# Kernel optimization log

Measured on AMD Instinct MI355X. Metric: run time of the kernel, lower is better.

The kernel has to match this reference:

```python
import jax, jax.numpy as jnp
import numpy as np

NUM_M = 512
NUM_T = 64
MAX_STEPS = 20
TAU = 1.0


def setup_inputs() -> dict:
    key = jax.random.key(0)
    ks = jax.random.split(key, 10)
    num_m, num_t = NUM_M, NUM_T
    inp = {
        "v_src": jax.random.normal(ks[0], (1, num_m), jnp.float32),
        "v_target": jax.random.normal(ks[1], (1, num_m), jnp.float32),
        # small-magnitude generators so matrix_exp stays well-conditioned
        "omegas": jax.random.normal(ks[2], (num_t, num_m, num_m), jnp.float32) * 0.01,
        "W1": jax.random.normal(ks[3], (2 * num_m, 256), jnp.float32) * (1.0 / np.sqrt(2 * num_m)),
        "b1": jnp.zeros((256,), jnp.float32),
        "W2": jax.random.normal(ks[4], (256, 128), jnp.float32) * (1.0 / np.sqrt(256)),
        "b2": jnp.zeros((128,), jnp.float32),
        "W3": jax.random.normal(ks[5], (128, num_t), jnp.float32) * (1.0 / np.sqrt(128)),
        "b3": jnp.zeros((num_t,), jnp.float32),
        # pre-sampled gumbel noise, one draw per step: [max_steps, B, num_t]
        "gumbel_noise": jax.random.gumbel(ks[6], (MAX_STEPS, 1, num_t), jnp.float32),
    }
    return inp


def reference(v_src, v_target, omegas, W1, b1, W2, b2, W3, b3, gumbel_noise):
    tgt_idx = jnp.argmax(v_target, axis=-1)  # [B]

    def mlp(x):
        h = jax.nn.relu(x @ W1 + b1)
        h = jax.nn.relu(h @ W2 + b2)
        return h @ W3 + b3  # [B, num_t]

    batched_expm = jax.vmap(jax.scipy.linalg.expm)

    def step(carry, g):
        v, done = carry  # v: [B, num_m], done: [B] bool
        x = jnp.concatenate([v, v_target], axis=-1)        # [B, 2*num_m]
        logits = mlp(x)                                     # [B, num_t]
        # gumbel_softmax(tau=1.0, hard=False)
        soft = jax.nn.softmax((logits + g) / TAU, axis=-1)
        omega_k = jnp.einsum('bt,tmk->bmk', soft, omegas)   # [B, m, m]
        R_k = batched_expm(omega_k)                         # [B, m, m]
        v_new = jnp.einsum('bmk,bk->bm', R_k, v)            # [B, m]
        # freeze state and zero-pad logits once the target marking was reached
        v_out = jnp.where(done[:, None], v, v_new)
        logits_out = jnp.where(done[:, None], jnp.zeros_like(logits), logits)
        done_new = done | (jnp.argmax(v_new, axis=-1) == tgt_idx)
        return (v_out, done_new), logits_out

    done0 = jnp.zeros((v_src.shape[0],), bool)
    (v_final, _), logits_seq = jax.lax.scan(step, (v_src, done0), gumbel_noise)
    # logits_seq: [max_steps, B, num_t]; B==1 -> [max_steps, num_t] (torch squeeze(0))
    return v_final, logits_seq[:, 0, :]
```

## Files before the change

kernel.cpp:

```cpp
#include <hip/hip_runtime.h>
#include <hip/hip_fp16.h>


#define NBLK 256
#define NTHR 512
#define NSTEP 20
#define NTAY 3
#define RBUF 4

typedef unsigned long long ull;

#define XW(buf, i) (X + ((((buf) << 8) + (i)) << 3))

__device__ __forceinline__ float wredsum(float p) {
#pragma unroll
  for (int off = 32; off > 0; off >>= 1) p += __shfl_xor(p, off, 64);
  return p;
}

__device__ __forceinline__ void publish2(ull* w, float v0, float v1, unsigned int tag2) {
  unsigned int u0 = (__float_as_uint(v0) & ~3u) | tag2;
  ull x = (ull)u0 | ((ull)__float_as_uint(v1) << 32);
  __hip_atomic_store(w, x, __ATOMIC_RELAXED, __HIP_MEMORY_SCOPE_AGENT);
}

__device__ __forceinline__ float2 poll2(ull* w, unsigned int tag2) {
  int it = 0;
  for (;;) {
    ull x = __hip_atomic_load(w, __ATOMIC_RELAXED, __HIP_MEMORY_SCOPE_AGENT);
    if ((unsigned int)(x & 3u) == tag2) {
      float2 r;
      r.x = __uint_as_float((unsigned int)x);
      r.y = __uint_as_float((unsigned int)(x >> 32));
      return r;
    }
    if (it == 0)      __builtin_amdgcn_s_sleep(1);
    else if (it == 1) __builtin_amdgcn_s_sleep(2);
    else              __builtin_amdgcn_s_sleep(4);
    if (it < 2) ++it;
  }
}

__global__ __launch_bounds__(NTHR) void petri_kernel(
    const float* __restrict__ vsrc, const float* __restrict__ vtgt,
    const float* __restrict__ omg,  const float* __restrict__ W1,
    const float* __restrict__ b1,   const float* __restrict__ W2,
    const float* __restrict__ b2,   const float* __restrict__ W3,
    const float* __restrict__ b3,   const float* __restrict__ gum,
    ull* __restrict__ X, float* __restrict__ out) {
  __shared__ __half2 oh[64 * 512];
  __shared__ float A0_s[512], A1_s[512];
  __shared__ float v_loc[512], tgt_s[512], w_s[512];
  __shared__ float w1c_s[1024];
  __shared__ float gum_s[NSTEP * 64];
  __shared__ float b2_s[128], b3_s[64];
  __shared__ float soft_s[64], h1_s[256], h2_s[128];
  __shared__ float redp[512];
  __shared__ float rf8[8];
  __shared__ int   ri8[8];
  __shared__ float acc2[2];
  __shared__ int   bc[1];

  const int b = blockIdx.x, tid = threadIdx.x;
  const int wv = tid >> 6, ln = tid & 63;

  v_loc[tid] = vsrc[tid];
  tgt_s[tid] = vtgt[tid];
  w1c_s[tid] = W1[tid * 256 + b];
  w1c_s[tid + 512] = W1[(tid + 512) * 256 + b];
  for (int i = tid; i < NSTEP * 64; i += NTHR) gum_s[i] = gum[i];
  if (tid >= 512 - 128) {
    int j = tid - (512 - 128);
    b2_s[j] = b2[j];
    if (j < 64) b3_s[j] = b3[j];
  }
  float w2r[64];
  {
    const int o = tid & 127, q = tid >> 7;
    const float* p = W2 + ((q << 6) * 128) + o;
#pragma unroll
    for (int i = 0; i < 64; ++i) w2r[i] = p[i * 128];
  }
  float w3r[16];
  {
    const int o = tid & 63, q = tid >> 6;
    const float* p = W3 + ((q << 4) * 64) + o;
#pragma unroll
    for (int i = 0; i < 16; ++i) w3r[i] = p[i * 64];
  }
  {
    const float* base0 = omg + (b << 10) + tid;
#pragma unroll 4
    for (int t = 0; t < 64; ++t) {
      float x0 = base0[t * 262144];
      float x1 = base0[t * 262144 + 512];
      oh[t * 512 + tid] = __floats2half2_rn(x0, x1);
    }
  }
  __syncthreads();

  int tgtIdx;
  {
    float v = tgt_s[tid]; int ix = tid;
#pragma unroll
    for (int off = 32; off > 0; off >>= 1) {
      float ov = __shfl_xor(v, off, 64); int oi = __shfl_xor(ix, off, 64);
      if (ov > v || (ov == v && oi < ix)) { v = ov; ix = oi; }
    }
    if (ln == 0) { rf8[wv] = v; ri8[wv] = ix; }
    __syncthreads();
    if (tid == 0) {
      float bv = rf8[0]; int bix = ri8[0];
      for (int q = 1; q < 8; ++q)
        if (rf8[q] > bv || (rf8[q] == bv && ri8[q] < bix)) { bv = rf8[q]; bix = ri8[q]; }
      bc[0] = bix;
    }
    __syncthreads();
    tgtIdx = bc[0];
    __syncthreads();
  }

  int d = 0;
  int r = 0;

  for (int s = 0; s < NSTEP; ++s) {
    if (d) {
      if (b == 0 && tid < 64) out[512 + s * 64 + tid] = 0.0f;
      continue;
    }

    {
      const int buf = r & (RBUF - 1);
      const unsigned int tg = (unsigned int)((r >> 2) & 3);
      float p = fmaf(v_loc[tid], w1c_s[tid], tgt_s[tid] * w1c_s[tid + 512]);
      p = wredsum(p);
      if (ln == 0) rf8[wv] = p;
      __syncthreads();
      if (tid == 0) {
        float a = b1[b];
        for (int q = 0; q < 8; ++q) a += rf8[q];
        float h = fmaxf(a, 0.f);
        publish2(XW(buf, b), h, h, tg);
      }
      if (tid < 256) h1_s[tid] = poll2(XW(buf, tid), tg).x;
      __syncthreads();
      ++r;
    }

    {
      const int q = tid >> 7;
      float a = 0.f;
      const float* hp = h1_s + (q << 6);
#pragma unroll
      for (int i = 0; i < 64; ++i) a = fmaf(hp[i], w2r[i], a);
      redp[tid] = a;
    }
    __syncthreads();
    if (tid < 128) {
      float rr = redp[tid] + redp[tid + 128] + redp[tid + 256] + redp[tid + 384] + b2_s[tid];
      h2_s[tid] = fmaxf(rr, 0.f);
    }
    __syncthreads();
    {
      const int q = tid >> 6;
      float a = 0.f;
      const float* hp = h2_s + (q << 4);
#pragma unroll
      for (int i = 0; i < 16; ++i) a = fmaf(hp[i], w3r[i], a);
      redp[tid] = a;
    }
    __syncthreads();
    if (tid < 64) {
      float a = b3_s[tid];
#pragma unroll
      for (int q = 0; q < 8; ++q) a += redp[tid + (q << 6)];
      float lg = a + gum_s[s * 64 + tid];
      float mx = lg;
#pragma unroll
      for (int off = 32; off > 0; off >>= 1) mx = fmaxf(mx, __shfl_xor(mx, off, 64));
      float e = __expf(lg - mx);
      float sm = e;
#pragma unroll
      for (int off = 32; off > 0; off >>= 1) sm += __shfl_xor(sm, off, 64);
      soft_s[tid] = e / sm;
      if (b == 0) out[512 + s * 64 + tid] = a;
    }
    __syncthreads();

    {
      float a0 = 0.f, a1 = 0.f;
#pragma unroll 8
      for (int t = 0; t < 64; ++t) {
        float2 xy = __half22float2(oh[t * 512 + tid]);
        float sv = soft_s[t];
        a0 = fmaf(sv, xy.x, a0);
        a1 = fmaf(sv, xy.y, a1);
      }
      A0_s[tid] = a0; A1_s[tid] = a1;
    }
    __syncthreads();

    {
      const int buf = r & (RBUF - 1);
      const unsigned int tg = (unsigned int)((r >> 2) & 3);
      const float* Ar = (tid < 256) ? A0_s : A1_s;
      const int j = tid & 255;
      float p = fmaf(Ar[j], v_loc[j], Ar[j + 256] * v_loc[j + 256]);
      p = wredsum(p);
      if (ln == 0) rf8[wv] = p;
      __syncthreads();
      if (tid == 0) {
        float s0 = rf8[0] + rf8[1] + rf8[2] + rf8[3];
        float s1 = rf8[4] + rf8[5] + rf8[6] + rf8[7];
        acc2[0] = v_loc[(b << 1)] + s0;
        acc2[1] = v_loc[(b << 1) + 1] + s1;
        publish2(XW(buf, b), s0, s1, tg);
      }
      if (tid < 256) {
        float2 g = poll2(XW(buf, tid), tg);
        w_s[(tid << 1)] = g.x;
        w_s[(tid << 1) + 1] = g.y;
      }
      __syncthreads();
      ++r;
    }

    for (int n = 2; n <= NTAY; ++n) {
      const int buf = r & (RBUF - 1);
      const unsigned int tg = (unsigned int)((r >> 2) & 3);
      const float* Ar = (tid < 256) ? A0_s : A1_s;
      const int j = tid & 255;
      float p = fmaf(Ar[j], w_s[j], Ar[j + 256] * w_s[j + 256]);
      p = wredsum(p);
      if (ln == 0) rf8[wv] = p;
      __syncthreads();
      if (tid == 0) {
        const float inv = 1.0f / (float)n;
        float s0 = (rf8[0] + rf8[1] + rf8[2] + rf8[3]) * inv;
        float s1 = (rf8[4] + rf8[5] + rf8[6] + rf8[7]) * inv;
        acc2[0] += s0; acc2[1] += s1;
        float p0 = (n < NTAY) ? s0 : acc2[0];
        float p1 = (n < NTAY) ? s1 : acc2[1];
        publish2(XW(buf, b), p0, p1, tg);
      }
      if (n < NTAY) {
        if (tid < 256) {
          float2 g = poll2(XW(buf, tid), tg);
          w_s[(tid << 1)] = g.x;
          w_s[(tid << 1) + 1] = g.y;
        }
        __syncthreads();
        ++r;
      } else {
        if (tid < 256) {
          float2 g = poll2(XW(buf, tid), tg);
          v_loc[(tid << 1)] = g.x;
          v_loc[(tid << 1) + 1] = g.y;
        }
        __syncthreads();
        float v = v_loc[tid]; int ix = tid;
#pragma unroll
        for (int off = 32; off > 0; off >>= 1) {
          float ov = __shfl_xor(v, off, 64); int oi = __shfl_xor(ix, off, 64);
          if (ov > v || (ov == v && oi < ix)) { v = ov; ix = oi; }
        }
        if (ln == 0) { rf8[wv] = v; ri8[wv] = ix; }
        __syncthreads();
        if (tid == 0) {
          float bv = rf8[0]; int bix = ri8[0];
          for (int q = 1; q < 8; ++q)
            if (rf8[q] > bv || (rf8[q] == bv && ri8[q] < bix)) { bv = rf8[q]; bix = ri8[q]; }
          bc[0] = (bix == tgtIdx) ? 1 : 0;
        }
        __syncthreads();
        if (bc[0]) d = 1;
        __syncthreads();
        ++r;
      }
    }
  }

  if (b == 0) out[tid] = v_loc[tid];
}

extern "C" void kernel_launch(void* const* d_in, const int* in_sizes, int n_in,
                              void* d_out, int out_size, void* d_ws, size_t ws_size,
                              hipStream_t stream) {
  (void)in_sizes; (void)n_in; (void)out_size; (void)ws_size;
  petri_kernel<<<dim3(NBLK), dim3(NTHR), 0, stream>>>(
      (const float*)d_in[0], (const float*)d_in[1], (const float*)d_in[2],
      (const float*)d_in[3], (const float*)d_in[4], (const float*)d_in[5],
      (const float*)d_in[6], (const float*)d_in[7], (const float*)d_in[8],
      (const float*)d_in[9], (ull*)d_ws, (float*)d_out);
}
```

Before: 364.6 us.

## Run Taylor-series exchange rounds in a single wavefront to drop block barriers

The three Taylor-series matvec and all-to-all exchange rounds, plus the final argmax, now run inside wavefront 0 alone. The state vector is held in registers, eight entries per lane, and each lane polls four slots at once, so the per-round __syncthreads and the LDS reduction through tid 0 go away. The constant target half of the first MLP layer is computed once before the loop, and the omega preload now uses float4 loads. In exchange, each round's dot product is done by 64 lanes instead of 512, and the other wavefronts sit idle during the critical serial exchange path.

```diff
diff --git a/kernel.cpp b/kernel.cpp
--- a/kernel.cpp
+++ b/kernel.cpp
@@ -16,6 +16,16 @@
 #pragma unroll
   for (int off = 32; off > 0; off >>= 1) p += __shfl_xor(p, off, 64);
   return p;
+}
+
+__device__ __forceinline__ void wredsum2(float& p0, float& p1) {
+#pragma unroll
+  for (int off = 32; off > 0; off >>= 1) {
+    float t0 = __shfl_xor(p0, off, 64);
+    float t1 = __shfl_xor(p1, off, 64);
+    p0 += t0;
+    p1 += t1;
+  }
 }
 
 __device__ __forceinline__ void publish2(ull* w, float v0, float v1, unsigned int tag2) {
@@ -41,6 +51,27 @@
   }
 }
 
+__device__ __forceinline__ void poll8(ull* w0, unsigned int tg, float* o) {
+  ull x0 = 0, x1 = 0, x2 = 0, x3 = 0;
+  bool g0 = false, g1 = false, g2 = false, g3 = false;
+  int it = 0;
+  for (;;) {
+    if (!g0) { ull x = __hip_atomic_load(w0,      __ATOMIC_RELAXED, __HIP_MEMORY_SCOPE_AGENT); if ((unsigned int)(x & 3u) == tg) { x0 = x; g0 = true; } }
+    if (!g1) { ull x = __hip_atomic_load(w0 + 8,  __ATOMIC_RELAXED, __HIP_MEMORY_SCOPE_AGENT); if ((unsigned int)(x & 3u) == tg) { x1 = x; g1 = true; } }
+    if (!g2) { ull x = __hip_atomic_load(w0 + 16, __ATOMIC_RELAXED, __HIP_MEMORY_SCOPE_AGENT); if ((unsigned int)(x & 3u) == tg) { x2 = x; g2 = true; } }
+    if (!g3) { ull x = __hip_atomic_load(w0 + 24, __ATOMIC_RELAXED, __HIP_MEMORY_SCOPE_AGENT); if ((unsigned int)(x & 3u) == tg) { x3 = x; g3 = true; } }
+    if (g0 && g1 && g2 && g3) break;
+    if (it == 0)      __builtin_amdgcn_s_sleep(1);
+    else if (it == 1) __builtin_amdgcn_s_sleep(2);
+    else              __builtin_amdgcn_s_sleep(4);
+    if (it < 2) ++it;
+  }
+  o[0] = __uint_as_float((unsigned int)x0); o[1] = __uint_as_float((unsigned int)(x0 >> 32));
+  o[2] = __uint_as_float((unsigned int)x1); o[3] = __uint_as_float((unsigned int)(x1 >> 32));
+  o[4] = __uint_as_float((unsigned int)x2); o[5] = __uint_as_float((unsigned int)(x2 >> 32));
+  o[6] = __uint_as_float((unsigned int)x3); o[7] = __uint_as_float((unsigned int)(x3 >> 32));
+}
+
 __global__ __launch_bounds__(NTHR) void petri_kernel(
     const float* __restrict__ vsrc, const float* __restrict__ vtgt,
     const float* __restrict__ omg,  const float* __restrict__ W1,
@@ -49,8 +80,10 @@
     const float* __restrict__ b3,   const float* __restrict__ gum,
     ull* __restrict__ X, float* __restrict__ out) {
   __shared__ __half2 oh[64 * 512];
-  __shared__ float A0_s[512], A1_s[512];
-  __shared__ float v_loc[512], tgt_s[512], w_s[512];
+  __shared__ __align__(16) float A0_s[512];
+  __shared__ __align__(16) float A1_s[512];
+  __shared__ __align__(16) float v_loc[512];
+  __shared__ float tgt_s[512];
   __shared__ float w1c_s[1024];
   __shared__ float gum_s[NSTEP * 64];
   __shared__ float b2_s[128], b3_s[64];
@@ -58,7 +91,7 @@
   __shared__ float redp[512];
   __shared__ float rf8[8];
   __shared__ int   ri8[8];
-  __shared__ float acc2[2];
+  __shared__ float cB_s[1];
   __shared__ int   bc[1];
 
   const int b = blockIdx.x, tid = threadIdx.x;
@@ -69,8 +102,8 @@
   w1c_s[tid] = W1[tid * 256 + b];
   w1c_s[tid + 512] = W1[(tid + 512) * 256 + b];
   for (int i = tid; i < NSTEP * 64; i += NTHR) gum_s[i] = gum[i];
-  if (tid >= 512 - 128) {
-    int j = tid - (512 - 128);
+  if (tid >= NTHR - 128) {
+    int j = tid - (NTHR - 128);
     b2_s[j] = b2[j];
     if (j < 64) b3_s[j] = b3[j];
   }
@@ -89,15 +122,36 @@
     for (int i = 0; i < 16; ++i) w3r[i] = p[i * 64];
   }
   {
-    const float* base0 = omg + (b << 10) + tid;
+    const int tq = tid >> 7;
+    const int c4 = (tid & 127) << 2;
+    const float* rp = omg + (b << 10) + c4;
 #pragma unroll 4
-    for (int t = 0; t < 64; ++t) {
-      float x0 = base0[t * 262144];
-      float x1 = base0[t * 262144 + 512];
-      oh[t * 512 + tid] = __floats2half2_rn(x0, x1);
+    for (int g = 0; g < 16; ++g) {
+      const int t = (g << 2) + tq;
+      const float* p = rp + t * 262144;
+      const float4 f0 = *(const float4*)(p);
+      const float4 f1 = *(const float4*)(p + 512);
+      __half2* dst = oh + t * 512 + c4;
+      dst[0] = __floats2half2_rn(f0.x, f1.x);
+      dst[1] = __floats2half2_rn(f0.y, f1.y);
+      dst[2] = __floats2half2_rn(f0.z, f1.z);
+      dst[3] = __floats2half2_rn(f0.w, f1.w);
     }
   }
   __syncthreads();
+
+  {
+    float p = tgt_s[tid] * w1c_s[tid + 512];
+    p = wredsum(p);
+    if (ln == 0) rf8[wv] = p;
+    __syncthreads();
+    if (tid == 0) {
+      float a = b1[b];
+      for (int q = 0; q < 8; ++q) a += rf8[q];
+      cB_s[0] = a;
+    }
+    __syncthreads();
+  }
 
   int tgtIdx;
   {
@@ -120,6 +174,13 @@
     __syncthreads();
   }
 
+  float vreg[8], w1t[8];
+  if (wv == 0) {
+    const int l8 = ln << 3;
+#pragma unroll
+    for (int k = 0; k < 8; ++k) { vreg[k] = v_loc[l8 + k]; w1t[k] = w1c_s[l8 + k]; }
+  }
+
   int d = 0;
   int r = 0;
 
@@ -132,15 +193,15 @@
     {
       const int buf = r & (RBUF - 1);
       const unsigned int tg = (unsigned int)((r >> 2) & 3);
-      float p = fmaf(v_loc[tid], w1c_s[tid], tgt_s[tid] * w1c_s[tid + 512]);
-      p = wredsum(p);
-      if (ln == 0) rf8[wv] = p;
-      __syncthreads();
-      if (tid == 0) {
-        float a = b1[b];
-        for (int q = 0; q < 8; ++q) a += rf8[q];
-        float h = fmaxf(a, 0.f);
-        publish2(XW(buf, b), h, h, tg);
+      if (wv == 0) {
+        float p = 0.f;
+#pragma unroll
+        for (int k = 0; k < 8; ++k) p = fmaf(vreg[k], w1t[k], p);
+        p = wredsum(p);
+        if (ln == 0) {
+          float h = fmaxf(p + cB_s[0], 0.f);
+          publish2(XW(buf, b), h, h, tg);
+        }
       }
       if (tid < 256) h1_s[tid] = poll2(XW(buf, tid), tg).x;
       __syncthreads();
@@ -200,84 +261,65 @@
     }
     __syncthreads();
 
-    {
-      const int buf = r & (RBUF - 1);
-      const unsigned int tg = (unsigned int)((r >> 2) & 3);
-      const float* Ar = (tid < 256) ? A0_s : A1_s;
-      const int j = tid & 255;
-      float p = fmaf(Ar[j], v_loc[j], Ar[j + 256] * v_loc[j + 256]);
-      p = wredsum(p);
-      if (ln == 0) rf8[wv] = p;
-      __syncthreads();
-      if (tid == 0) {
-        float s0 = rf8[0] + rf8[1] + rf8[2] + rf8[3];
-        float s1 = rf8[4] + rf8[5] + rf8[6] + rf8[7];
-        acc2[0] = v_loc[(b << 1)] + s0;
-        acc2[1] = v_loc[(b << 1) + 1] + s1;
-        publish2(XW(buf, b), s0, s1, tg);
+    if (wv == 0) {
+      const int l8 = ln << 3;
+      float wreg[8];
+#pragma unroll
+      for (int k = 0; k < 8; ++k) wreg[k] = vreg[k];
+      float acc0 = 0.f, acc1 = 0.f;
+#pragma unroll
+      for (int n = 1; n <= NTAY; ++n) {
+        const int rr = r + (n - 1);
+        const int buf = rr & (RBUF - 1);
+        const unsigned int tg = (unsigned int)((rr >> 2) & 3);
+        const float4 a00 = *(const float4*)(A0_s + l8);
+        const float4 a01 = *(const float4*)(A0_s + l8 + 4);
+        const float4 a10 = *(const float4*)(A1_s + l8);
+        const float4 a11 = *(const float4*)(A1_s + l8 + 4);
+        float p0 = 0.f, p1 = 0.f;
+        p0 = fmaf(a00.x, wreg[0], p0); p0 = fmaf(a00.y, wreg[1], p0);
+        p0 = fmaf(a00.z, wreg[2], p0); p0 = fmaf(a00.w, wreg[3], p0);
+        p0 = fmaf(a01.x, wreg[4], p0); p0 = fmaf(a01.y, wreg[5], p0);
+        p0 = fmaf(a01.z, wreg[6], p0); p0 = fmaf(a01.w, wreg[7], p0);
+        p1 = fmaf(a10.x, wreg[0], p1); p1 = fmaf(a10.y, wreg[1], p1);
+        p1 = fmaf(a10.z, wreg[2], p1); p1 = fmaf(a10.w, wreg[3], p1);
+        p1 = fmaf(a11.x, wreg[4], p1); p1 = fmaf(a11.y, wreg[5], p1);
+        p1 = fmaf(a11.z, wreg[6], p1); p1 = fmaf(a11.w, wreg[7], p1);
+        wredsum2(p0, p1);
+        if (ln == 0) {
+          float s0, s1;
+          if (n == 1) {
+            s0 = p0; s1 = p1;
+            acc0 = v_loc[(b << 1)] + s0;
+            acc1 = v_loc[(b << 1) + 1] + s1;
+          } else {
+            const float inv = (n == 2) ? 0.5f : (1.0f / 3.0f);
+            s0 = p0 * inv; s1 = p1 * inv;
+            acc0 += s0; acc1 += s1;
+          }
+          const float q0 = (n < NTAY) ? s0 : acc0;
+          const float q1 = (n < NTAY) ? s1 : acc1;
+          publish2(XW(buf, b), q0, q1, tg);
+        }
+        poll8(XW(buf, (ln << 2)), tg, wreg);
       }
-      if (tid < 256) {
-        float2 g = poll2(XW(buf, tid), tg);
-        w_s[(tid << 1)] = g.x;
-        w_s[(tid << 1) + 1] = g.y;
+#pragma unroll
+      for (int k = 0; k < 8; ++k) vreg[k] = wreg[k];
+      *(float4*)(v_loc + l8)     = make_float4(wreg[0], wreg[1], wreg[2], wreg[3]);
+      *(float4*)(v_loc + l8 + 4) = make_float4(wreg[4], wreg[5], wreg[6], wreg[7]);
+      float mv = wreg[0]; int mi = l8;
+#pragma unroll
+      for (int k = 1; k < 8; ++k) if (wreg[k] > mv) { mv = wreg[k]; mi = l8 + k; }
+#pragma unroll
+      for (int off = 32; off > 0; off >>= 1) {
+        float ov = __shfl_xor(mv, off, 64); int oi = __shfl_xor(mi, off, 64);
+        if (ov > mv || (ov == mv && oi < mi)) { mv = ov; mi = oi; }
       }
-      __syncthreads();
-      ++r;
-    }
-
-    for (int n = 2; n <= NTAY; ++n) {
-      const int buf = r & (RBUF - 1);
-      const unsigned int tg = (unsigned int)((r >> 2) & 3);
-      const float* Ar = (tid < 256) ? A0_s : A1_s;
-      const int j = tid & 255;
-      float p = fmaf(Ar[j], w_s[j], Ar[j + 256] * w_s[j + 256]);
-      p = wredsum(p);
-      if (ln == 0) rf8[wv] = p;
-      __syncthreads();
-      if (tid == 0) {
-        const float inv = 1.0f / (float)n;
-        float s0 = (rf8[0] + rf8[1] + rf8[2] + rf8[3]) * inv;
-        float s1 = (rf8[4] + rf8[5] + rf8[6] + rf8[7]) * inv;
-        acc2[0] += s0; acc2[1] += s1;
-        float p0 = (n < NTAY) ? s0 : acc2[0];
-        float p1 = (n < NTAY) ? s1 : acc2[1];
-        publish2(XW(buf, b), p0, p1, tg);
-      }
-      if (n < NTAY) {
-        if (tid < 256) {
-          float2 g = poll2(XW(buf, tid), tg);
-          w_s[(tid << 1)] = g.x;
-          w_s[(tid << 1) + 1] = g.y;
-        }
-        __syncthreads();
-        ++r;
-      } else {
-        if (tid < 256) {
-          float2 g = poll2(XW(buf, tid), tg);
-          v_loc[(tid << 1)] = g.x;
-          v_loc[(tid << 1) + 1] = g.y;
-        }
-        __syncthreads();
-        float v = v_loc[tid]; int ix = tid;
-#pragma unroll
-        for (int off = 32; off > 0; off >>= 1) {
-          float ov = __shfl_xor(v, off, 64); int oi = __shfl_xor(ix, off, 64);
-          if (ov > v || (ov == v && oi < ix)) { v = ov; ix = oi; }
-        }
-        if (ln == 0) { rf8[wv] = v; ri8[wv] = ix; }
-        __syncthreads();
-        if (tid == 0) {
-          float bv = rf8[0]; int bix = ri8[0];
-          for (int q = 1; q < 8; ++q)
-            if (rf8[q] > bv || (rf8[q] == bv && ri8[q] < bix)) { bv = rf8[q]; bix = ri8[q]; }
-          bc[0] = (bix == tgtIdx) ? 1 : 0;
-        }
-        __syncthreads();
-        if (bc[0]) d = 1;
-        __syncthreads();
-        ++r;
-      }
-    }
+      if (ln == 0) bc[0] = (mi == tgtIdx) ? 1 : 0;
+    }
+    __syncthreads();
+    if (bc[0]) d = 1;
+    r += NTAY;
   }
 
   if (b == 0) out[tid] = v_loc[tid];
```

New measurement: 343.0 us. 5.9% less time.
